# Optimization experiments

Hardware: AMD Instinct MI355X
Metric: run time of the kernel (lower is better)

Reference implementation:

```python
import jax, jax.numpy as jnp
import numpy as np


def setup_inputs() -> dict:
    key = jax.random.key(0)
    k1, k2, k3 = jax.random.split(key, 3)
    B, Lq, Lk, D = 8, 512, 512, 64
    q = jax.random.normal(k1, (B, Lq, D), dtype=jnp.float32)
    k = jax.random.normal(k2, (B, Lk, D), dtype=jnp.float32)
    v = jax.random.normal(k3, (B, Lk, D), dtype=jnp.float32)
    return {"q": q, "k": k, "v": v}


def reference(q, k, v):
    scale = 1.0
    # broadcast add: [B, Lq, 1, D] + [B, 1, Lk, D] -> [B, Lq, Lk, D]
    scores = jnp.sum(scale * jnp.tanh(q[:, :, None, :] + k[:, None, :, :]), axis=-1)  # [B, Lq, Lk]
    attn = jax.nn.softmax(scores, axis=-1)
    out = jnp.einsum('bqk,bkd->bqd', attn, v)
    return out
```

## Files before the change

### kernel.cpp

```cpp
#include <hip/hip_runtime.h>

namespace {
constexpr int Bn = 8, LQ = 512, LK = 512, Dn = 64;
constexpr int T = 512, QT = 8, KT = 256, NT = LK / KT;
constexpr float C2 = 2.8853900817779268f;

__global__ __launch_bounds__(T, 4)
void addattn(const float* __restrict__ Q, const float* __restrict__ K,
             const float* __restrict__ V, float* __restrict__ O)
{
  __shared__ __align__(16) float ek[KT][Dn + 1];
  __shared__ __align__(16) float eqs[QT][Dn];
  __shared__ __align__(16) float pl[QT][KT + 4];
  __shared__ float lsum[QT];

  const int t  = threadIdx.x;
  const int bb = blockIdx.x >> 6;
  const int q0 = (blockIdx.x & 63) * QT;

  if (t < 128) {
    const int r = t >> 4, d4 = t & 15;
    float4 qv = *(const float4*)(Q + ((bb * LQ + q0 + r) * Dn) + d4 * 4);
    float4 e;
    e.x = __builtin_amdgcn_exp2f(qv.x * C2);
    e.y = __builtin_amdgcn_exp2f(qv.y * C2);
    e.z = __builtin_amdgcn_exp2f(qv.z * C2);
    e.w = __builtin_amdgcn_exp2f(qv.w * C2);
    *(float4*)&eqs[r][d4 * 4] = e;
  }
  if (t < QT) lsum[t] = 0.f;

  const int sk_ = t >> 4, sd_ = t & 15;
  float4 kv[8];
  const float* kbase = K + (bb * LK) * Dn + sd_ * 4;

  #pragma unroll
  for (int p = 0; p < 8; ++p)
    kv[p] = *(const float4*)(kbase + (p * 32 + sk_) * Dn);
  #pragma unroll
  for (int p = 0; p < 8; ++p) {
    const int row = p * 32 + sk_;
    ek[row][sd_ * 4 + 0] = __builtin_amdgcn_exp2f(kv[p].x * C2);
    ek[row][sd_ * 4 + 1] = __builtin_amdgcn_exp2f(kv[p].y * C2);
    ek[row][sd_ * 4 + 2] = __builtin_amdgcn_exp2f(kv[p].z * C2);
    ek[row][sd_ * 4 + 3] = __builtin_amdgcn_exp2f(kv[p].w * C2);
  }
  __syncthreads();

  const int kk = t & 255;
  const int qb = (t >> 8) * 4;
  const int dq  = t & 15;
  const int rg  = (t >> 4) & 3;
  const int seg = t >> 6;
  float ac00 = 0.f, ac01 = 0.f, ac02 = 0.f, ac03 = 0.f;
  float ac10 = 0.f, ac11 = 0.f, ac12 = 0.f, ac13 = 0.f;

  for (int tile = 0; tile < NT; ++tile) {
    const int k0 = tile * KT;

    if (tile + 1 < NT) {
      #pragma unroll
      for (int p = 0; p < 8; ++p)
        kv[p] = *(const float4*)(kbase + (k0 + KT + p * 32 + sk_) * Dn);
    }

    {
      float a0 = 0.f, a1 = 0.f, a2 = 0.f, a3 = 0.f;
      #pragma unroll
      for (int d4 = 0; d4 < 16; ++d4) {
        const float4 e0 = *(const float4*)&eqs[qb + 0][d4 * 4];
        const float4 e1 = *(const float4*)&eqs[qb + 1][d4 * 4];
        const float4 e2 = *(const float4*)&eqs[qb + 2][d4 * 4];
        const float4 e3 = *(const float4*)&eqs[qb + 3][d4 * 4];
        const float x0 = ek[kk][d4 * 4 + 0];
        const float x1 = ek[kk][d4 * 4 + 1];
        const float x2 = ek[kk][d4 * 4 + 2];
        const float x3 = ek[kk][d4 * 4 + 3];
        a0 += __builtin_amdgcn_rcpf(fmaf(e0.x, x0, 1.f));
        a1 += __builtin_amdgcn_rcpf(fmaf(e1.x, x0, 1.f));
        a2 += __builtin_amdgcn_rcpf(fmaf(e2.x, x0, 1.f));
        a3 += __builtin_amdgcn_rcpf(fmaf(e3.x, x0, 1.f));
        a0 += __builtin_amdgcn_rcpf(fmaf(e0.y, x1, 1.f));
        a1 += __builtin_amdgcn_rcpf(fmaf(e1.y, x1, 1.f));
        a2 += __builtin_amdgcn_rcpf(fmaf(e2.y, x1, 1.f));
        a3 += __builtin_amdgcn_rcpf(fmaf(e3.y, x1, 1.f));
        a0 += __builtin_amdgcn_rcpf(fmaf(e0.z, x2, 1.f));
        a1 += __builtin_amdgcn_rcpf(fmaf(e1.z, x2, 1.f));
        a2 += __builtin_amdgcn_rcpf(fmaf(e2.z, x2, 1.f));
        a3 += __builtin_amdgcn_rcpf(fmaf(e3.z, x2, 1.f));
        a0 += __builtin_amdgcn_rcpf(fmaf(e0.w, x3, 1.f));
        a1 += __builtin_amdgcn_rcpf(fmaf(e1.w, x3, 1.f));
        a2 += __builtin_amdgcn_rcpf(fmaf(e2.w, x3, 1.f));
        a3 += __builtin_amdgcn_rcpf(fmaf(e3.w, x3, 1.f));
      }
      const float p0 = __builtin_amdgcn_exp2f(-C2 * a0);
      const float p1 = __builtin_amdgcn_exp2f(-C2 * a1);
      const float p2 = __builtin_amdgcn_exp2f(-C2 * a2);
      const float p3 = __builtin_amdgcn_exp2f(-C2 * a3);
      pl[qb + 0][kk] = p0;
      pl[qb + 1][kk] = p1;
      pl[qb + 2][kk] = p2;
      pl[qb + 3][kk] = p3;

      float s0 = p0, s1 = p1, s2 = p2, s3 = p3;
      #pragma unroll
      for (int m = 1; m < 64; m <<= 1) {
        s0 += __shfl_xor(s0, m);
        s1 += __shfl_xor(s1, m);
        s2 += __shfl_xor(s2, m);
        s3 += __shfl_xor(s3, m);
      }
      if ((t & 63) == 0) {
        atomicAdd(&lsum[qb + 0], s0);
        atomicAdd(&lsum[qb + 1], s1);
        atomicAdd(&lsum[qb + 2], s2);
        atomicAdd(&lsum[qb + 3], s3);
      }
    }
    __syncthreads();

    {
      const float* vb   = V + ((bb * LK + k0 + seg * 32) * Dn) + dq * 4;
      const float* pr0  = &pl[2 * rg + 0][seg * 32];
      const float* pr1  = &pl[2 * rg + 1][seg * 32];
      #pragma unroll 8
      for (int j = 0; j < 32; ++j) {
        float4 v4 = *(const float4*)(vb + j * Dn);
        float pa = pr0[j], pb = pr1[j];
        ac00 = fmaf(pa, v4.x, ac00);
        ac01 = fmaf(pa, v4.y, ac01);
        ac02 = fmaf(pa, v4.z, ac02);
        ac03 = fmaf(pa, v4.w, ac03);
        ac10 = fmaf(pb, v4.x, ac10);
        ac11 = fmaf(pb, v4.y, ac11);
        ac12 = fmaf(pb, v4.z, ac12);
        ac13 = fmaf(pb, v4.w, ac13);
      }
    }

    if (tile + 1 < NT) {
      #pragma unroll
      for (int p = 0; p < 8; ++p) {
        const int row = p * 32 + sk_;
        ek[row][sd_ * 4 + 0] = __builtin_amdgcn_exp2f(kv[p].x * C2);
        ek[row][sd_ * 4 + 1] = __builtin_amdgcn_exp2f(kv[p].y * C2);
        ek[row][sd_ * 4 + 2] = __builtin_amdgcn_exp2f(kv[p].z * C2);
        ek[row][sd_ * 4 + 3] = __builtin_amdgcn_exp2f(kv[p].w * C2);
      }
    }
    __syncthreads();
  }

  float* scr = &ek[0][0];
  *(float4*)(scr + ((seg * 8 + 2 * rg + 0) * 64) + dq * 4) =
      make_float4(ac00, ac01, ac02, ac03);
  *(float4*)(scr + ((seg * 8 + 2 * rg + 1) * 64) + dq * 4) =
      make_float4(ac10, ac11, ac12, ac13);
  __syncthreads();
  if (t < 128) {
    const int row = t >> 4, d4 = t & 15;
    float4 o = make_float4(0.f, 0.f, 0.f, 0.f);
    #pragma unroll
    for (int s = 0; s < 8; ++s) {
      float4 c = *(const float4*)(scr + ((s * 8 + row) * 64) + d4 * 4);
      o.x += c.x; o.y += c.y; o.z += c.z; o.w += c.w;
    }
    const float inv = 1.0f / lsum[row];
    o.x *= inv; o.y *= inv; o.z *= inv; o.w *= inv;
    *(float4*)(O + ((bb * LQ + q0 + row) * Dn) + d4 * 4) = o;
  }
}
}

extern "C" void kernel_launch(void* const* d_in, const int* in_sizes, int n_in,
                              void* d_out, int out_size, void* d_ws, size_t ws_size,
                              hipStream_t stream) {
  (void)in_sizes; (void)n_in; (void)d_ws; (void)ws_size; (void)out_size;
  const float* Q = (const float*)d_in[0];
  const float* K = (const float*)d_in[1];
  const float* V = (const float*)d_in[2];
  float* O = (float*)d_out;
  addattn<<<dim3(Bn * (LQ / QT)), dim3(T), 0, stream>>>(Q, K, V, O);
}
```

Baseline: 95.90 us.

## Shrink key tile to 128, prefetch V into registers, split score accumulators

New measurement: 85.01 us. -11.4%, faster.

```diff
diff --git a/kernel.cpp b/kernel.cpp
--- a/kernel.cpp
+++ b/kernel.cpp
@@ -2,14 +2,14 @@
 
 namespace {
 constexpr int Bn = 8, LQ = 512, LK = 512, Dn = 64;
-constexpr int T = 512, QT = 8, KT = 256, NT = LK / KT;
+constexpr int T = 512, QT = 8, KT = 128, NT = LK / KT;
 constexpr float C2 = 2.8853900817779268f;
 
 __global__ __launch_bounds__(T, 4)
 void addattn(const float* __restrict__ Q, const float* __restrict__ K,
              const float* __restrict__ V, float* __restrict__ O)
 {
-  __shared__ __align__(16) float ek[KT][Dn + 1];
+  __shared__ __align__(16) float ek[KT][66];
   __shared__ __align__(16) float eqs[QT][Dn];
   __shared__ __align__(16) float pl[QT][KT + 4];
   __shared__ float lsum[QT];
@@ -17,6 +17,15 @@
   const int t  = threadIdx.x;
   const int bb = blockIdx.x >> 6;
   const int q0 = (blockIdx.x & 63) * QT;
+
+  const int sk_ = t >> 4, sd_ = t & 15;
+  const int kk = t & 127;
+  const int qg = (t >> 7) * 2;
+  const int dq  = t & 15;
+  const int rg  = (t >> 4) & 3;
+  const int seg = t >> 6;
+
+  const float* kbase = K + (bb * LK) * Dn + sd_ * 4;
 
   if (t < 128) {
     const int r = t >> 4, d4 = t & 15;
@@ -30,15 +39,12 @@
   }
   if (t < QT) lsum[t] = 0.f;
 
-  const int sk_ = t >> 4, sd_ = t & 15;
-  float4 kv[8];
-  const float* kbase = K + (bb * LK) * Dn + sd_ * 4;
-
+  float4 kv[4];
   #pragma unroll
-  for (int p = 0; p < 8; ++p)
+  for (int p = 0; p < 4; ++p)
     kv[p] = *(const float4*)(kbase + (p * 32 + sk_) * Dn);
   #pragma unroll
-  for (int p = 0; p < 8; ++p) {
+  for (int p = 0; p < 4; ++p) {
     const int row = p * 32 + sk_;
     ek[row][sd_ * 4 + 0] = __builtin_amdgcn_exp2f(kv[p].x * C2);
     ek[row][sd_ * 4 + 1] = __builtin_amdgcn_exp2f(kv[p].y * C2);
@@ -47,100 +53,83 @@
   }
   __syncthreads();
 
-  const int kk = t & 255;
-  const int qb = (t >> 8) * 4;
-  const int dq  = t & 15;
-  const int rg  = (t >> 4) & 3;
-  const int seg = t >> 6;
   float ac00 = 0.f, ac01 = 0.f, ac02 = 0.f, ac03 = 0.f;
   float ac10 = 0.f, ac11 = 0.f, ac12 = 0.f, ac13 = 0.f;
 
   for (int tile = 0; tile < NT; ++tile) {
     const int k0 = tile * KT;
 
+    float4 vv[16];
+    {
+      const float* vbase = V + ((bb * LK + k0 + seg * 16) * Dn) + dq * 4;
+      #pragma unroll
+      for (int j = 0; j < 16; ++j)
+        vv[j] = *(const float4*)(vbase + j * Dn);
+    }
     if (tile + 1 < NT) {
       #pragma unroll
-      for (int p = 0; p < 8; ++p)
+      for (int p = 0; p < 4; ++p)
         kv[p] = *(const float4*)(kbase + (k0 + KT + p * 32 + sk_) * Dn);
     }
 
     {
-      float a0 = 0.f, a1 = 0.f, a2 = 0.f, a3 = 0.f;
+      float a0 = 0.f, b0 = 0.f, a1 = 0.f, b1 = 0.f;
+      const float* ekr = &ek[kk][0];
+      const float* eq0 = &eqs[qg + 0][0];
+      const float* eq1 = &eqs[qg + 1][0];
       #pragma unroll
       for (int d4 = 0; d4 < 16; ++d4) {
-        const float4 e0 = *(const float4*)&eqs[qb + 0][d4 * 4];
-        const float4 e1 = *(const float4*)&eqs[qb + 1][d4 * 4];
-        const float4 e2 = *(const float4*)&eqs[qb + 2][d4 * 4];
-        const float4 e3 = *(const float4*)&eqs[qb + 3][d4 * 4];
-        const float x0 = ek[kk][d4 * 4 + 0];
-        const float x1 = ek[kk][d4 * 4 + 1];
-        const float x2 = ek[kk][d4 * 4 + 2];
-        const float x3 = ek[kk][d4 * 4 + 3];
-        a0 += __builtin_amdgcn_rcpf(fmaf(e0.x, x0, 1.f));
-        a1 += __builtin_amdgcn_rcpf(fmaf(e1.x, x0, 1.f));
-        a2 += __builtin_amdgcn_rcpf(fmaf(e2.x, x0, 1.f));
-        a3 += __builtin_amdgcn_rcpf(fmaf(e3.x, x0, 1.f));
-        a0 += __builtin_amdgcn_rcpf(fmaf(e0.y, x1, 1.f));
-        a1 += __builtin_amdgcn_rcpf(fmaf(e1.y, x1, 1.f));
-        a2 += __builtin_amdgcn_rcpf(fmaf(e2.y, x1, 1.f));
-        a3 += __builtin_amdgcn_rcpf(fmaf(e3.y, x1, 1.f));
-        a0 += __builtin_amdgcn_rcpf(fmaf(e0.z, x2, 1.f));
-        a1 += __builtin_amdgcn_rcpf(fmaf(e1.z, x2, 1.f));
-        a2 += __builtin_amdgcn_rcpf(fmaf(e2.z, x2, 1.f));
-        a3 += __builtin_amdgcn_rcpf(fmaf(e3.z, x2, 1.f));
-        a0 += __builtin_amdgcn_rcpf(fmaf(e0.w, x3, 1.f));
-        a1 += __builtin_amdgcn_rcpf(fmaf(e1.w, x3, 1.f));
-        a2 += __builtin_amdgcn_rcpf(fmaf(e2.w, x3, 1.f));
-        a3 += __builtin_amdgcn_rcpf(fmaf(e3.w, x3, 1.f));
+        const float4 e0 = *(const float4*)(eq0 + d4 * 4);
+        const float4 e1 = *(const float4*)(eq1 + d4 * 4);
+        const float2 xA = *(const float2*)(ekr + d4 * 4);
+        const float2 xB = *(const float2*)(ekr + d4 * 4 + 2);
+        a0 += __builtin_amdgcn_rcpf(fmaf(e0.x, xA.x, 1.f));
+        b0 += __builtin_amdgcn_rcpf(fmaf(e0.y, xA.y, 1.f));
+        a0 += __builtin_amdgcn_rcpf(fmaf(e0.z, xB.x, 1.f));
+        b0 += __builtin_amdgcn_rcpf(fmaf(e0.w, xB.y, 1.f));
+        a1 += __builtin_amdgcn_rcpf(fmaf(e1.x, xA.x, 1.f));
+        b1 += __builtin_amdgcn_rcpf(fmaf(e1.y, xA.y, 1.f));
+        a1 += __builtin_amdgcn_rcpf(fmaf(e1.z, xB.x, 1.f));
+        b1 += __builtin_amdgcn_rcpf(fmaf(e1.w, xB.y, 1.f));
       }
-      const float p0 = __builtin_amdgcn_exp2f(-C2 * a0);
-      const float p1 = __builtin_amdgcn_exp2f(-C2 * a1);
-      const float p2 = __builtin_amdgcn_exp2f(-C2 * a2);
-      const float p3 = __builtin_amdgcn_exp2f(-C2 * a3);
-      pl[qb + 0][kk] = p0;
-      pl[qb + 1][kk] = p1;
-      pl[qb + 2][kk] = p2;
-      pl[qb + 3][kk] = p3;
+      const float p0 = __builtin_amdgcn_exp2f(-C2 * (a0 + b0));
+      const float p1 = __builtin_amdgcn_exp2f(-C2 * (a1 + b1));
+      pl[qg + 0][kk] = p0;
+      pl[qg + 1][kk] = p1;
 
-      float s0 = p0, s1 = p1, s2 = p2, s3 = p3;
+      float s0 = p0, s1 = p1;
       #pragma unroll
       for (int m = 1; m < 64; m <<= 1) {
         s0 += __shfl_xor(s0, m);
         s1 += __shfl_xor(s1, m);
-        s2 += __shfl_xor(s2, m);
-        s3 += __shfl_xor(s3, m);
       }
       if ((t & 63) == 0) {
-        atomicAdd(&lsum[qb + 0], s0);
-        atomicAdd(&lsum[qb + 1], s1);
-        atomicAdd(&lsum[qb + 2], s2);
-        atomicAdd(&lsum[qb + 3], s3);
+        atomicAdd(&lsum[qg + 0], s0);
+        atomicAdd(&lsum[qg + 1], s1);
       }
     }
     __syncthreads();
 
     {
-      const float* vb   = V + ((bb * LK + k0 + seg * 32) * Dn) + dq * 4;
-      const float* pr0  = &pl[2 * rg + 0][seg * 32];
-      const float* pr1  = &pl[2 * rg + 1][seg * 32];
-      #pragma unroll 8
-      for (int j = 0; j < 32; ++j) {
-        float4 v4 = *(const float4*)(vb + j * Dn);
-        float pa = pr0[j], pb = pr1[j];
-        ac00 = fmaf(pa, v4.x, ac00);
-        ac01 = fmaf(pa, v4.y, ac01);
-        ac02 = fmaf(pa, v4.z, ac02);
-        ac03 = fmaf(pa, v4.w, ac03);
-        ac10 = fmaf(pb, v4.x, ac10);
-        ac11 = fmaf(pb, v4.y, ac11);
-        ac12 = fmaf(pb, v4.z, ac12);
-        ac13 = fmaf(pb, v4.w, ac13);
+      const float* pr0 = &pl[2 * rg + 0][seg * 16];
+      const float* pr1 = &pl[2 * rg + 1][seg * 16];
+      #pragma unroll
+      for (int j = 0; j < 16; ++j) {
+        const float pa = pr0[j], pb = pr1[j];
+        ac00 = fmaf(pa, vv[j].x, ac00);
+        ac01 = fmaf(pa, vv[j].y, ac01);
+        ac02 = fmaf(pa, vv[j].z, ac02);
+        ac03 = fmaf(pa, vv[j].w, ac03);
+        ac10 = fmaf(pb, vv[j].x, ac10);
+        ac11 = fmaf(pb, vv[j].y, ac11);
+        ac12 = fmaf(pb, vv[j].z, ac12);
+        ac13 = fmaf(pb, vv[j].w, ac13);
       }
     }
 
     if (tile + 1 < NT) {
       #pragma unroll
-      for (int p = 0; p < 8; ++p) {
+      for (int p = 0; p < 4; ++p) {
         const int row = p * 32 + sk_;
         ek[row][sd_ * 4 + 0] = __builtin_amdgcn_exp2f(kv[p].x * C2);
         ek[row][sd_ * 4 + 1] = __builtin_amdgcn_exp2f(kv[p].y * C2);
```
